# Kernel optimization log

Measured on AMD Instinct MI355X. Metric: run time of the kernel, lower is better.

The kernel has to match this reference:

```python
import jax, jax.numpy as jnp
import numpy as np

B, S, D_MODEL, H = 4, 4096, 1024, 16
HD = D_MODEL // H  # 64
KS = 3             # depthwise conv kernel size
EPS = 1e-6


def dw_causal_conv(x, w, b):
    """Causal depthwise conv over seq. x: [B,S,H,Dk], w: [Dk,KS], b: [Dk].
    Matches Conv1d(groups=d_k, padding=KS-1) followed by cropping the last KS-1."""
    s = x.shape[1]
    xp = jnp.pad(x, ((0, 0), (KS - 1, 0), (0, 0), (0, 0)))
    y = b  # broadcast over [B,S,H,Dk]
    for j in range(KS):
        y = y + w[:, j] * xp[:, j:j + s]
    return y


def feature_map(x):
    return jax.nn.elu(x) + 1.0


def setup_inputs() -> dict:
    key = jax.random.key(0)
    ks = jax.random.split(key, 20)
    sc = 0.02
    inp = {
        'query': jax.random.normal(ks[0], (B, S, D_MODEL), jnp.float32),
        'key':   jax.random.normal(ks[1], (B, S, D_MODEL), jnp.float32),
        'value': jax.random.normal(ks[2], (B, S, D_MODEL), jnp.float32),
        'q_w': jax.random.normal(ks[3], (D_MODEL, D_MODEL), jnp.float32) * sc,
        'q_b': jax.random.normal(ks[4], (D_MODEL,), jnp.float32) * sc,
        'k_w': jax.random.normal(ks[5], (D_MODEL, D_MODEL), jnp.float32) * sc,
        'k_b': jax.random.normal(ks[6], (D_MODEL,), jnp.float32) * sc,
        'v_w': jax.random.normal(ks[7], (D_MODEL, D_MODEL), jnp.float32) * sc,
        'v_b': jax.random.normal(ks[8], (D_MODEL,), jnp.float32) * sc,
        'o_w': jax.random.normal(ks[9], (D_MODEL, D_MODEL), jnp.float32) * sc,
        'o_b': jax.random.normal(ks[10], (D_MODEL,), jnp.float32) * sc,
        'qc_w': jax.random.normal(ks[11], (HD, KS), jnp.float32) * 0.3,
        'qc_b': jax.random.normal(ks[12], (HD,), jnp.float32) * 0.02,
        'kc_w': jax.random.normal(ks[13], (HD, KS), jnp.float32) * 0.3,
        'kc_b': jax.random.normal(ks[14], (HD,), jnp.float32) * 0.02,
        'vc_w': jax.random.normal(ks[15], (HD, KS), jnp.float32) * 0.3,
        'vc_b': jax.random.normal(ks[16], (HD,), jnp.float32) * 0.02,
    }
    return inp


def reference(query, key, value, q_w, q_b, k_w, k_b, v_w, v_b, o_w, o_b,
              qc_w, qc_b, kc_w, kc_b, vc_w, vc_b):
    b, s, _ = query.shape
    q = (query @ q_w.T + q_b).reshape(b, s, H, HD)
    k = (key   @ k_w.T + k_b).reshape(b, s, H, HD)
    v = (value @ v_w.T + v_b).reshape(b, s, H, HD)

    q = feature_map(dw_causal_conv(q, qc_w, qc_b))
    k = feature_map(dw_causal_conv(k, kc_w, kc_b))
    v = dw_causal_conv(v, vc_w, vc_b)

    # linear attention: [B,S,H,D] -> [B,H,S,D]
    Q = q.transpose(0, 2, 1, 3)
    K = k.transpose(0, 2, 1, 3)
    V = v.transpose(0, 2, 1, 3)
    KV = jnp.einsum('bhsd,bhse->bhde', K, V)            # [B,H,D,D]
    Z = 1.0 / jnp.einsum('bhsd,bhd->bhs', Q, K.sum(axis=2) + EPS)
    V_new = jnp.einsum('bhde,bhsd,bhs->bhse', KV, Q, Z)  # [B,H,S,D]

    out = V_new.transpose(0, 2, 1, 3).reshape(b, s, D_MODEL)
    return out @ o_w.T + o_b
```

## Files before the change

### kernel.cpp

```cpp
#include <hip/hip_runtime.h>
#include <hip/hip_bf16.h>
#include <math.h>

#define BB 4
#define SS 4096
#define DM 1024
#define HH 16
#define HD 64
#define NTOK (BB * SS)
#define TSZ ((size_t)NTOK * DM)

typedef _Float16 half8 __attribute__((ext_vector_type(8)));
typedef _Float16 half4v __attribute__((ext_vector_type(4)));
typedef float floatx4 __attribute__((ext_vector_type(4)));

__device__ __forceinline__ void gload16(const void* g, void* l) {
  __builtin_amdgcn_global_load_lds(
      (const __attribute__((address_space(1))) void*)g,
      (__attribute__((address_space(3))) void*)l, 16, 0, 0);
}

#define WAIT4 asm volatile("s_waitcnt vmcnt(4)" ::: "memory")
#define WAIT2 asm volatile("s_waitcnt vmcnt(2)" ::: "memory")
#define WAIT0 asm volatile("s_waitcnt vmcnt(0)" ::: "memory")
#define BARR __builtin_amdgcn_s_barrier()

#define MM3(A_, ah_, al_, bh_, bl_)                                   \
  A_ = __builtin_amdgcn_mfma_f32_16x16x32_f16(ah_, bh_, A_, 0, 0, 0); \
  A_ = __builtin_amdgcn_mfma_f32_16x16x32_f16(ah_, bl_, A_, 0, 0, 0); \
  A_ = __builtin_amdgcn_mfma_f32_16x16x32_f16(al_, bh_, A_, 0, 0, 0)

__device__ __forceinline__ void cvhl(const float4 u0, const float4 u1,
                                     half8& h, half8& l) {
  const float a[8] = {u0.x, u0.y, u0.z, u0.w, u1.x, u1.y, u1.z, u1.w};
#pragma unroll
  for (int e = 0; e < 8; ++e) {
    const _Float16 hh = (_Float16)a[e];
    h[e] = hh;
    l[e] = (_Float16)(a[e] - (float)hh);
  }
}

__global__ __launch_bounds__(256) void split_w4(
    const float* __restrict__ w0, const float* __restrict__ w1,
    const float* __restrict__ w2, const float* __restrict__ w3,
    _Float16* __restrict__ hi, _Float16* __restrict__ lo) {
  const int wi = blockIdx.y;
  const float* src = (wi == 0) ? w0 : (wi == 1) ? w1 : (wi == 2) ? w2 : w3;
  const int i = blockIdx.x * 256 + threadIdx.x;
  const size_t off = ((size_t)wi << 20) >> 2;
  const float4 x = ((const float4*)src)[i];
  half4v h, l;
  h.x = (_Float16)x.x; l.x = (_Float16)(x.x - (float)h.x);
  h.y = (_Float16)x.y; l.y = (_Float16)(x.y - (float)h.y);
  h.z = (_Float16)x.z; l.z = (_Float16)(x.z - (float)h.z);
  h.w = (_Float16)x.w; l.w = (_Float16)(x.w - (float)h.w);
  ((half4v*)hi)[off + i] = h;
  ((half4v*)lo)[off + i] = l;
}

__global__ __launch_bounds__(512, 2) void qkv_gemm8(
    const float* __restrict__ Ak, const float* __restrict__ Av,
    const float* __restrict__ Aq, const _Float16* __restrict__ WhiA,
    const _Float16* __restrict__ WloA, const float* __restrict__ bk,
    const float* __restrict__ bv, const float* __restrict__ bq,
    float* __restrict__ Ck, float* __restrict__ Cv, float* __restrict__ Cq) {
  __shared__ float sA[2][256 * 32];
  __shared__ _Float16 sB[2][256 * 64];

  const int z = blockIdx.z;
  const float* A = (z == 0) ? Ak : (z == 1) ? Av : Aq;
  const float* bias = (z == 0) ? bk : (z == 1) ? bv : bq;
  float* C = (z == 0) ? Ck : (z == 1) ? Cv : Cq;
  const _Float16* Whi = WhiA + ((size_t)z << 20);
  const _Float16* Wlo = WloA + ((size_t)z << 20);

  const int t = threadIdx.x;
  const int wav = t >> 6, lane = t & 63;
  const int wr = wav >> 2, wc = wav & 3;

  const int wg = blockIdx.y * 4 + blockIdx.x;
  const int xcd = wg & 7, cidx = wg >> 3;
  const int bm = ((xcd >> 1) * 16 + (cidx >> 1)) * 256;
  const int bn = ((xcd & 1) * 2 + (cidx & 1)) * 256;

  const int lrow = wav * 8 + (lane >> 3);
  const int cpr = (lane & 7) ^ (lane >> 3);
  const float* pA0 = A + (size_t)(bm + lrow) * DM + cpr * 4;
  const _Float16* pB0 =
      ((cpr < 4) ? Whi : Wlo) + (size_t)(bn + lrow) * DM + (cpr & 3) * 8;
  const int ldsArow = wav * 8 * 32;
  const int ldsBrow = wav * 8 * 64;

#define STA(buf, rb, k0) \
  gload16(pA0 + (size_t)(rb) * DM + (k0), &sA[buf][(rb) * 32 + ldsArow])
#define STB(buf, rb, k0) \
  gload16(pB0 + (size_t)(rb) * DM + (k0), &sB[buf][(rb) * 64 + ldsBrow])

  STA(0, 0, 0); STA(0, 64, 0);
  STB(0, 0, 0); STB(0, 64, 0);
  STB(0, 128, 0); STB(0, 192, 0);
  STA(0, 128, 0); STA(0, 192, 0);

  const int fm = lane & 15;
  const int sw = fm & 7;
  const int kq = lane >> 4;
  int baseA[4], baseB[2];
#pragma unroll
  for (int i = 0; i < 4; ++i) baseA[i] = (wr * 64 + i * 16 + fm) * 32;
#pragma unroll
  for (int j = 0; j < 2; ++j) baseB[j] = (wc * 32 + j * 16 + fm) * 64;
  const int aS0 = ((kq * 2) ^ sw) * 4;
  const int aS1 = ((kq * 2 + 1) ^ sw) * 4;
  const int bSh = (kq ^ sw) * 8;
  const int bSl = ((kq + 4) ^ sw) * 8;

  floatx4 acc[2][4][2][2];
#pragma unroll
  for (int i = 0; i < 2; ++i)
#pragma unroll
    for (int j = 0; j < 4; ++j)
#pragma unroll
      for (int k = 0; k < 2; ++k)
#pragma unroll
        for (int l = 0; l < 2; ++l)
          acc[i][j][k][l] = (floatx4){0.f, 0.f, 0.f, 0.f};

  half8 ah[4], al[4];
  half8 b0h0, b0l0, b0h1, b0l1;
  half8 b1h0, b1l0, b1h1, b1l1;

#define READA_Q(cur_, QM)                                       \
  _Pragma("unroll") for (int i_ = 0; i_ < 4; ++i_) {            \
    const float4 u0_ =                                          \
        *(const float4*)&sA[cur_][baseA[i_] + (QM) * 4096 + aS0]; \
    const float4 u1_ =                                          \
        *(const float4*)&sA[cur_][baseA[i_] + (QM) * 4096 + aS1]; \
    cvhl(u0_, u1_, ah[i_], al[i_]);                             \
  }

#define RB_Q(cur_, QN, H0, L0, H1, L1)                          \
  H0 = *(const half8*)&sB[cur_][baseB[0] + (QN) * 8192 + bSh];  \
  L0 = *(const half8*)&sB[cur_][baseB[0] + (QN) * 8192 + bSl];  \
  H1 = *(const half8*)&sB[cur_][baseB[1] + (QN) * 8192 + bSh];  \
  L1 = *(const half8*)&sB[cur_][baseB[1] + (QN) * 8192 + bSl]

#define MFMACL(QM, QN, H0, L0, H1, L1)                          \
  __builtin_amdgcn_s_setprio(1);                                \
  _Pragma("unroll") for (int i_ = 0; i_ < 4; ++i_) {            \
    MM3(acc[QM][i_][QN][0], ah[i_], al[i_], H0, L0);            \
    MM3(acc[QM][i_][QN][1], ah[i_], al[i_], H1, L1);            \
  }                                                             \
  __builtin_amdgcn_s_setprio(0)

  for (int tt = 0; tt < 31; ++tt) {
    const int cur = tt & 1, nxt = cur ^ 1;
    const int k1 = tt * 32 + 32;
    WAIT4; BARR;
    READA_Q(cur, 0);
    RB_Q(cur, 0, b0h0, b0l0, b0h1, b0l1);
    STA(nxt, 0, k1); STA(nxt, 64, k1);
    MFMACL(0, 0, b0h0, b0l0, b0h1, b0l1);
    BARR;
    WAIT4; BARR;
    RB_Q(cur, 1, b1h0, b1l0, b1h1, b1l1);
    STB(nxt, 0, k1); STB(nxt, 64, k1);
    MFMACL(0, 1, b1h0, b1l0, b1h1, b1l1);
    BARR;
    WAIT4; BARR;
    READA_Q(cur, 1);
    STB(nxt, 128, k1); STB(nxt, 192, k1);
    MFMACL(1, 0, b0h0, b0l0, b0h1, b0l1);
    BARR;
    STA(nxt, 128, k1); STA(nxt, 192, k1);
    MFMACL(1, 1, b1h0, b1l0, b1h1, b1l1);
  }
  WAIT4; BARR;
  READA_Q(1, 0);
  RB_Q(1, 0, b0h0, b0l0, b0h1, b0l1);
  MFMACL(0, 0, b0h0, b0l0, b0h1, b0l1);
  BARR;
  WAIT2; BARR;
  RB_Q(1, 1, b1h0, b1l0, b1h1, b1l1);
  MFMACL(0, 1, b1h0, b1l0, b1h1, b1l1);
  BARR;
  WAIT0; BARR;
  READA_Q(1, 1);
  MFMACL(1, 0, b0h0, b0l0, b0h1, b0l1);
  MFMACL(1, 1, b1h0, b1l0, b1h1, b1l1);

  const int cr = (lane >> 4) * 4;
#pragma unroll
  for (int qm = 0; qm < 2; ++qm)
#pragma unroll
    for (int i = 0; i < 4; ++i) {
      const int grow = bm + qm * 128 + wr * 64 + i * 16 + cr;
#pragma unroll
      for (int qn = 0; qn < 2; ++qn)
#pragma unroll
        for (int j = 0; j < 2; ++j) {
          const int gcol = bn + qn * 128 + wc * 32 + j * 16 + fm;
          const float bo = bias[gcol];
#pragma unroll
          for (int r = 0; r < 4; ++r)
            C[(size_t)(grow + r) * DM + gcol] = acc[qm][i][qn][j][r] + bo;
        }
    }
#undef STA
#undef STB
#undef READA_Q
#undef RB_Q
#undef MFMACL
}

__global__ __launch_bounds__(512, 2) void o_gemm8(
    const _Float16* __restrict__ Ahi, const _Float16* __restrict__ Alo,
    const _Float16* __restrict__ Whi, const _Float16* __restrict__ Wlo,
    const float* __restrict__ bias, float* __restrict__ C) {
  __shared__ _Float16 sA[2][256 * 64];
  __shared__ _Float16 sB[2][256 * 64];

  const int t = threadIdx.x;
  const int wav = t >> 6, lane = t & 63;
  const int wr = wav >> 2, wc = wav & 3;

  const int wg = blockIdx.y * 4 + blockIdx.x;
  const int xcd = wg & 7, cidx = wg >> 3;
  const int bm = ((xcd >> 1) * 16 + (cidx >> 1)) * 256;
  const int bn = ((xcd & 1) * 2 + (cidx & 1)) * 256;

  const int lrow = wav * 8 + (lane >> 3);
  const int cpr = (lane & 7) ^ (lane >> 3);
  const _Float16* pA0 =
      ((cpr < 4) ? Ahi : Alo) + (size_t)(bm + lrow) * DM + (cpr & 3) * 8;
  const _Float16* pB0 =
      ((cpr < 4) ? Whi : Wlo) + (size_t)(bn + lrow) * DM + (cpr & 3) * 8;
  const int ldsRow = wav * 8 * 64;

#define STAO(buf, rb, k0) \
  gload16(pA0 + (size_t)(rb) * DM + (k0), &sA[buf][(rb) * 64 + ldsRow])
#define STBO(buf, rb, k0) \
  gload16(pB0 + (size_t)(rb) * DM + (k0), &sB[buf][(rb) * 64 + ldsRow])

  STAO(0, 0, 0); STAO(0, 64, 0);
  STBO(0, 0, 0); STBO(0, 64, 0);
  STBO(0, 128, 0); STBO(0, 192, 0);
  STAO(0, 128, 0); STAO(0, 192, 0);

  const int fm = lane & 15;
  const int sw = fm & 7;
  const int kq = lane >> 4;
  int baseA[4], baseB[2];
#pragma unroll
  for (int i = 0; i < 4; ++i) baseA[i] = (wr * 64 + i * 16 + fm) * 64;
#pragma unroll
  for (int j = 0; j < 2; ++j) baseB[j] = (wc * 32 + j * 16 + fm) * 64;
  const int bSh = (kq ^ sw) * 8;
  const int bSl = ((kq + 4) ^ sw) * 8;

  floatx4 acc[2][4][2][2];
#pragma unroll
  for (int i = 0; i < 2; ++i)
#pragma unroll
    for (int j = 0; j < 4; ++j)
#pragma unroll
      for (int k = 0; k < 2; ++k)
#pragma unroll
        for (int l = 0; l < 2; ++l)
          acc[i][j][k][l] = (floatx4){0.f, 0.f, 0.f, 0.f};

  half8 ah[4], al[4];
  half8 b0h0, b0l0, b0h1, b0l1;
  half8 b1h0, b1l0, b1h1, b1l1;

#define READA_O(cur_, QM)                                                 \
  _Pragma("unroll") for (int i_ = 0; i_ < 4; ++i_) {                      \
    ah[i_] = *(const half8*)&sA[cur_][baseA[i_] + (QM) * 8192 + bSh];     \
    al[i_] = *(const half8*)&sA[cur_][baseA[i_] + (QM) * 8192 + bSl];     \
  }

#define RB_O(cur_, QN, H0, L0, H1, L1)                          \
  H0 = *(const half8*)&sB[cur_][baseB[0] + (QN) * 8192 + bSh];  \
  L0 = *(const half8*)&sB[cur_][baseB[0] + (QN) * 8192 + bSl];  \
  H1 = *(const half8*)&sB[cur_][baseB[1] + (QN) * 8192 + bSh];  \
  L1 = *(const half8*)&sB[cur_][baseB[1] + (QN) * 8192 + bSl]

#define MFMACLO(QM, QN, H0, L0, H1, L1)                         \
  __builtin_amdgcn_s_setprio(1);                                \
  _Pragma("unroll") for (int i_ = 0; i_ < 4; ++i_) {            \
    MM3(acc[QM][i_][QN][0], ah[i_], al[i_], H0, L0);            \
    MM3(acc[QM][i_][QN][1], ah[i_], al[i_], H1, L1);            \
  }                                                             \
  __builtin_amdgcn_s_setprio(0)

  for (int tt = 0; tt < 31; ++tt) {
    const int cur = tt & 1, nxt = cur ^ 1;
    const int k1 = tt * 32 + 32;
    WAIT4; BARR;
    READA_O(cur, 0);
    RB_O(cur, 0, b0h0, b0l0, b0h1, b0l1);
    STAO(nxt, 0, k1); STAO(nxt, 64, k1);
    MFMACLO(0, 0, b0h0, b0l0, b0h1, b0l1);
    BARR;
    WAIT4; BARR;
    RB_O(cur, 1, b1h0, b1l0, b1h1, b1l1);
    STBO(nxt, 0, k1); STBO(nxt, 64, k1);
    MFMACLO(0, 1, b1h0, b1l0, b1h1, b1l1);
    BARR;
    WAIT4; BARR;
    READA_O(cur, 1);
    STBO(nxt, 128, k1); STBO(nxt, 192, k1);
    MFMACLO(1, 0, b0h0, b0l0, b0h1, b0l1);
    BARR;
    STAO(nxt, 128, k1); STAO(nxt, 192, k1);
    MFMACLO(1, 1, b1h0, b1l0, b1h1, b1l1);
  }
  WAIT4; BARR;
  READA_O(1, 0);
  RB_O(1, 0, b0h0, b0l0, b0h1, b0l1);
  MFMACLO(0, 0, b0h0, b0l0, b0h1, b0l1);
  BARR;
  WAIT2; BARR;
  RB_O(1, 1, b1h0, b1l0, b1h1, b1l1);
  MFMACLO(0, 1, b1h0, b1l0, b1h1, b1l1);
  BARR;
  WAIT0; BARR;
  READA_O(1, 1);
  MFMACLO(1, 0, b0h0, b0l0, b0h1, b0l1);
  MFMACLO(1, 1, b1h0, b1l0, b1h1, b1l1);

  const int cr = (lane >> 4) * 4;
#pragma unroll
  for (int qm = 0; qm < 2; ++qm)
#pragma unroll
    for (int i = 0; i < 4; ++i) {
      const int grow = bm + qm * 128 + wr * 64 + i * 16 + cr;
#pragma unroll
      for (int qn = 0; qn < 2; ++qn)
#pragma unroll
        for (int j = 0; j < 2; ++j) {
          const int gcol = bn + qn * 128 + wc * 32 + j * 16 + fm;
          const float bo = bias[gcol];
#pragma unroll
          for (int r = 0; r < 4; ++r)
            C[(size_t)(grow + r) * DM + gcol] = acc[qm][i][qn][j][r] + bo;
        }
    }
#undef STAO
#undef STBO
#undef READA_O
#undef RB_O
#undef MFMACLO
}

__global__ __launch_bounds__(256) void kv_accum_conv(
    const float* __restrict__ Kg, const float* __restrict__ Vg,
    const float* __restrict__ kc_w, const float* __restrict__ kc_b,
    const float* __restrict__ vc_w, const float* __restrict__ vc_b,
    float* __restrict__ KVp, float* __restrict__ Ksp) {
  const int bh = blockIdx.x;
  const int b = bh >> 4, h = bh & 15;
  const int chunk = blockIdx.y;
  const int s0 = chunk * 256;
  const int t = threadIdx.x;
  const int w = t >> 6, lane = t & 63;
  __shared__ float Kr[34][64], Vr[34][64];
  __shared__ float Kc[32][64], Vc[32][64];
  __shared__ float kw0[64], kw1[64], kw2[64], kb_[64];
  __shared__ float vw0[64], vw1[64], vw2[64], vb_[64];

  if (t < 64) {
    kw0[t] = kc_w[t * 3 + 0]; kw1[t] = kc_w[t * 3 + 1]; kw2[t] = kc_w[t * 3 + 2];
    vw0[t] = vc_w[t * 3 + 0]; vw1[t] = vc_w[t * 3 + 1]; vw2[t] = vc_w[t * 3 + 2];
    kb_[t] = kc_b[t]; vb_[t] = vc_b[t];
  }

  const int d0 = w * 16 + (lane >> 4) * 4;
  const int e0 = (lane & 15) * 4;
  float acc[4][4];
#pragma unroll
  for (int i = 0; i < 4; ++i)
#pragma unroll
    for (int j = 0; j < 4; ++j) acc[i][j] = 0.f;
  float4 ks = make_float4(0.f, 0.f, 0.f, 0.f);
  const size_t gbase = (size_t)b * SS * DM + h * HD;

  float4 kpre[3], vpre[3];
#define KVFETCH(cc)                                                        \
  _Pragma("unroll") for (int u = 0; u < 3; ++u) {                          \
    const int idx = t + u * 256;                                           \
    if (idx < 544) {                                                       \
      const int row = idx >> 4, col = (idx & 15) * 4;                      \
      const int s = s0 + (cc) - 2 + row;                                   \
      float4 k4 = make_float4(0.f, 0.f, 0.f, 0.f);                         \
      float4 v4 = make_float4(0.f, 0.f, 0.f, 0.f);                         \
      if (s >= 0) {                                                        \
        k4 = *(const float4*)&Kg[gbase + (size_t)s * DM + col];            \
        v4 = *(const float4*)&Vg[gbase + (size_t)s * DM + col];            \
      }                                                                    \
      kpre[u] = k4; vpre[u] = v4;                                          \
    }                                                                      \
  }
#define KVWRITE                                                            \
  _Pragma("unroll") for (int u = 0; u < 3; ++u) {                          \
    const int idx = t + u * 256;                                           \
    if (idx < 544) {                                                       \
      const int row = idx >> 4, col = (idx & 15) * 4;                      \
      *(float4*)&Kr[row][col] = kpre[u];                                   \
      *(float4*)&Vr[row][col] = vpre[u];                                   \
    }                                                                      \
  }

  KVFETCH(0);
  for (int c = 0; c < 256; c += 32) {
    __syncthreads();
    KVWRITE;
    __syncthreads();
    for (int idx = t; idx < 2048; idx += 256) {
      const int row = idx >> 6, dd = idx & 63;
      float yk = kb_[dd] + kw0[dd] * Kr[row][dd] + kw1[dd] * Kr[row + 1][dd] +
                 kw2[dd] * Kr[row + 2][dd];
      Kc[row][dd] = (yk > 0.f) ? (yk + 1.f) : expf(yk);
      Vc[row][dd] = vb_[dd] + vw0[dd] * Vr[row][dd] + vw1[dd] * Vr[row + 1][dd] +
                    vw2[dd] * Vr[row + 2][dd];
    }
    if (c + 32 < 256) KVFETCH(c + 32);
    __syncthreads();
#pragma unroll 2
    for (int ss = 0; ss < 32; ++ss) {
      const float4 k4 = *(const float4*)&Kc[ss][d0];
      const float4 v4 = *(const float4*)&Vc[ss][e0];
      ks.x += k4.x; ks.y += k4.y; ks.z += k4.z; ks.w += k4.w;
      const float kk[4] = {k4.x, k4.y, k4.z, k4.w};
      const float vv[4] = {v4.x, v4.y, v4.z, v4.w};
#pragma unroll
      for (int i = 0; i < 4; ++i)
#pragma unroll
        for (int j = 0; j < 4; ++j) acc[i][j] = fmaf(kk[i], vv[j], acc[i][j]);
    }
  }
  float* kvp = &KVp[((size_t)(bh * 16 + chunk)) * 4096];
#pragma unroll
  for (int i = 0; i < 4; ++i) {
    float4 o = make_float4(acc[i][0], acc[i][1], acc[i][2], acc[i][3]);
    *(float4*)&kvp[(d0 + i) * 64 + e0] = o;
  }
  if ((lane & 15) == 0) {
    float* kp = &Ksp[(bh * 16 + chunk) * 64 + d0];
    kp[0] = ks.x; kp[1] = ks.y; kp[2] = ks.z; kp[3] = ks.w;
  }
#undef KVFETCH
#undef KVWRITE
}

__global__ __launch_bounds__(256) void kv_reduce(
    const float* __restrict__ KVp, const float* __restrict__ Ksp,
    float* __restrict__ KV, float* __restrict__ Ksum) {
  const int bh = blockIdx.x;
  const int t = threadIdx.x;
  for (int i = t; i < 4096; i += 256) {
    float s = 0.f;
#pragma unroll
    for (int c = 0; c < 16; ++c) s += KVp[((size_t)(bh * 16 + c)) * 4096 + i];
    KV[(size_t)bh * 4096 + i] = s;
  }
  if (t < 64) {
    float s = 1e-6f;
#pragma unroll
    for (int c = 0; c < 16; ++c) s += Ksp[(bh * 16 + c) * 64 + t];
    Ksum[bh * 64 + t] = s;
  }
}

__global__ __launch_bounds__(256) void attn_apply_conv(
    const float* __restrict__ Qg, const float* __restrict__ KV,
    const float* __restrict__ Ksum, const float* __restrict__ qc_w,
    const float* __restrict__ qc_b, _Float16* __restrict__ OHi,
    _Float16* __restrict__ OLo) {
  const int bh = blockIdx.x;
  const int b = bh >> 4, h = bh & 15;
  const int s0 = blockIdx.y * 64;
  const int t = threadIdx.x;
  const int w = t >> 6, lane = t & 63;
  __shared__ float Qr[66][64];
  __shared__ float QsT[64][68];
  __shared__ float KVs[64][64];
  __shared__ float pden[64][4];
  __shared__ float kse[64];
  __shared__ float qw0[64], qw1[64], qw2[64], qb_[64];
  const size_t gbase = (size_t)b * SS * DM + h * HD;

  for (int idx = t; idx < 1056; idx += 256) {
    const int row = idx >> 4, col = (idx & 15) * 4;
    const int s = s0 - 2 + row;
    float4 q4 = make_float4(0.f, 0.f, 0.f, 0.f);
    if (s >= 0) q4 = *(const float4*)&Qg[gbase + (size_t)s * DM + col];
    *(float4*)&Qr[row][col] = q4;
  }
  for (int idx = t; idx < 1024; idx += 256) {
    const int row = idx >> 4, col = (idx & 15) * 4;
    *(float4*)&KVs[row][col] = *(const float4*)&KV[(size_t)bh * 4096 + row * 64 + col];
  }
  if (t < 64) {
    kse[t] = Ksum[bh * 64 + t];
    qw0[t] = qc_w[t * 3 + 0]; qw1[t] = qc_w[t * 3 + 1]; qw2[t] = qc_w[t * 3 + 2];
    qb_[t] = qc_b[t];
  }
  __syncthreads();

  {
    const int crow = t >> 2;
    const int db = (t & 3) * 16;
    float denp = 0.f;
#pragma unroll
    for (int q = 0; q < 4; ++q) {
      const float4 xm2 = *(const float4*)&Qr[crow][db + q * 4];
      const float4 xm1 = *(const float4*)&Qr[crow + 1][db + q * 4];
      const float4 xc0 = *(const float4*)&Qr[crow + 2][db + q * 4];
      const float a2[4] = {xm2.x, xm2.y, xm2.z, xm2.w};
      const float a1[4] = {xm1.x, xm1.y, xm1.z, xm1.w};
      const float a0[4] = {xc0.x, xc0.y, xc0.z, xc0.w};
#pragma unroll
      for (int e = 0; e < 4; ++e) {
        const int dd = db + q * 4 + e;
        float y = qb_[dd] + qw0[dd] * a2[e] + qw1[dd] * a1[e] + qw2[dd] * a0[e];
        y = (y > 0.f) ? (y + 1.f) : expf(y);
        denp = fmaf(y, kse[dd], denp);
        QsT[dd][crow] = y;
      }
    }
    pden[crow][t & 3] = denp;
  }
  __syncthreads();

  const int sl0 = w * 16 + (lane >> 4) * 4;
  const int e0 = (lane & 15) * 4;
  float acc[4][4];
#pragma unroll
  for (int i = 0; i < 4; ++i)
#pragma unroll
    for (int j = 0; j < 4; ++j) acc[i][j] = 0.f;
#pragma unroll 2
  for (int d = 0; d < 64; ++d) {
    const float4 q4 = *(const float4*)&QsT[d][sl0];
    const float4 v4 = *(const float4*)&KVs[d][e0];
    const float qq[4] = {q4.x, q4.y, q4.z, q4.w};
    const float vv[4] = {v4.x, v4.y, v4.z, v4.w};
#pragma unroll
    for (int i = 0; i < 4; ++i)
#pragma unroll
      for (int j = 0; j < 4; ++j) acc[i][j] = fmaf(qq[i], vv[j], acc[i][j]);
  }
#pragma unroll
  for (int i = 0; i < 4; ++i) {
    const float4 pd = *(const float4*)&pden[sl0 + i][0];
    const float zz = 1.0f / (pd.x + pd.y + pd.z + pd.w);
    const float o[4] = {acc[i][0] * zz, acc[i][1] * zz, acc[i][2] * zz,
                        acc[i][3] * zz};
    half4v hh, ll;
#pragma unroll
    for (int e = 0; e < 4; ++e) {
      const _Float16 hv = (_Float16)o[e];
      hh[e] = hv;
      ll[e] = (_Float16)(o[e] - (float)hv);
    }
    const size_t base = gbase + (size_t)(s0 + sl0 + i) * DM + e0;
    *(half4v*)&OHi[base] = hh;
    *(half4v*)&OLo[base] = ll;
  }
}

extern "C" void kernel_launch(void* const* d_in, const int* in_sizes, int n_in,
                              void* d_out, int out_size, void* d_ws, size_t ws_size,
                              hipStream_t stream) {
  const float* query = (const float*)d_in[0];
  const float* key   = (const float*)d_in[1];
  const float* value = (const float*)d_in[2];
  const float* q_w = (const float*)d_in[3];
  const float* q_b = (const float*)d_in[4];
  const float* k_w = (const float*)d_in[5];
  const float* k_b = (const float*)d_in[6];
  const float* v_w = (const float*)d_in[7];
  const float* v_b = (const float*)d_in[8];
  const float* o_w = (const float*)d_in[9];
  const float* o_b = (const float*)d_in[10];
  const float* qc_w = (const float*)d_in[11];
  const float* qc_b = (const float*)d_in[12];
  const float* kc_w = (const float*)d_in[13];
  const float* kc_b = (const float*)d_in[14];
  const float* vc_w = (const float*)d_in[15];
  const float* vc_b = (const float*)d_in[16];
  float* out = (float*)d_out;

  float* ws = (float*)d_ws;
  float* buf0 = ws;
  float* buf1 = ws + TSZ;
  float* buf2 = ws + 2 * TSZ;
  _Float16* Whi = (_Float16*)(ws + 3 * TSZ);
  _Float16* Wlo = Whi + 4 * (1 << 20);
  float* KVp  = (float*)(Wlo + 4 * (1 << 20));
  float* Ksp  = KVp + (size_t)64 * 16 * 4096;
  float* KV   = Ksp + 64 * 16 * 64;
  float* Ksum = KV + (size_t)64 * 4096;

  _Float16* WhiO = Whi + 3 * (1 << 20);
  _Float16* WloO = Wlo + 3 * (1 << 20);
  _Float16* OHi = (_Float16*)buf0;
  _Float16* OLo = OHi + TSZ;

  const int nW4 = DM * DM / 4;

  split_w4<<<dim3(nW4 / 256, 4), 256, 0, stream>>>(k_w, v_w, q_w, o_w, Whi, Wlo);

  qkv_gemm8<<<dim3(4, 64, 3), 512, 0, stream>>>(
      key, value, query, Whi, Wlo, k_b, v_b, q_b, buf0, buf1, buf2);

  kv_accum_conv<<<dim3(64, 16), 256, 0, stream>>>(buf0, buf1, kc_w, kc_b, vc_w,
                                                  vc_b, KVp, Ksp);
  kv_reduce<<<64, 256, 0, stream>>>(KVp, Ksp, KV, Ksum);

  attn_apply_conv<<<dim3(64, 64), 256, 0, stream>>>(buf2, KV, Ksum, qc_w, qc_b,
                                                    OHi, OLo);

  o_gemm8<<<dim3(4, 64), 512, 0, stream>>>(OHi, OLo, WhiO, WloO, o_b, out);
}
```

Measured before the change: 722.5 us.

## Simplify GEMM pipelining to one wait per k-step and drop KV register prefetch

Both fp16-split GEMMs replace the fine-grained interleaved staging, with partial vmcnt waits and several barriers per k-step, by one full wait and barrier. After that barrier all next-tile loads are issued at once, then the full MFMA cluster runs. The kv_accum_conv kernel drops its register prefetch of the next K/V chunk and loads it synchronously instead. This cuts barrier count and register pressure, but gives up finer overlap of global loads with compute and exposes load latency in the conv kernel.

```diff
diff --git a/kernel.cpp b/kernel.cpp
--- a/kernel.cpp
+++ b/kernel.cpp
@@ -20,8 +20,6 @@
       (__attribute__((address_space(3))) void*)l, 16, 0, 0);
 }
 
-#define WAIT4 asm volatile("s_waitcnt vmcnt(4)" ::: "memory")
-#define WAIT2 asm volatile("s_waitcnt vmcnt(2)" ::: "memory")
 #define WAIT0 asm volatile("s_waitcnt vmcnt(0)" ::: "memory")
 #define BARR __builtin_amdgcn_s_barrier()
 
@@ -59,7 +57,7 @@
   ((half4v*)lo)[off + i] = l;
 }
 
-__global__ __launch_bounds__(512, 2) void qkv_gemm8(
+__global__ __launch_bounds__(512, 2) void qkv_gemm9(
     const float* __restrict__ Ak, const float* __restrict__ Av,
     const float* __restrict__ Aq, const _Float16* __restrict__ WhiA,
     const _Float16* __restrict__ WloA, const float* __restrict__ bk,
@@ -97,10 +95,13 @@
 #define STB(buf, rb, k0) \
   gload16(pB0 + (size_t)(rb) * DM + (k0), &sB[buf][(rb) * 64 + ldsBrow])
 
-  STA(0, 0, 0); STA(0, 64, 0);
-  STB(0, 0, 0); STB(0, 64, 0);
-  STB(0, 128, 0); STB(0, 192, 0);
-  STA(0, 128, 0); STA(0, 192, 0);
+#define STAGE_ALL(buf, k0)                          \
+  STA(buf, 0, k0); STA(buf, 64, k0);                \
+  STA(buf, 128, k0); STA(buf, 192, k0);             \
+  STB(buf, 0, k0); STB(buf, 64, k0);                \
+  STB(buf, 128, k0); STB(buf, 192, k0)
+
+  STAGE_ALL(0, 0);
 
   const int fm = lane & 15;
   const int sw = fm & 7;
@@ -145,49 +146,36 @@
   H1 = *(const half8*)&sB[cur_][baseB[1] + (QN) * 8192 + bSh];  \
   L1 = *(const half8*)&sB[cur_][baseB[1] + (QN) * 8192 + bSl]
 
-#define MFMACL(QM, QN, H0, L0, H1, L1)                          \
+#define MFMACL(QM)                                              \
   __builtin_amdgcn_s_setprio(1);                                \
   _Pragma("unroll") for (int i_ = 0; i_ < 4; ++i_) {            \
-    MM3(acc[QM][i_][QN][0], ah[i_], al[i_], H0, L0);            \
-    MM3(acc[QM][i_][QN][1], ah[i_], al[i_], H1, L1);            \
+    MM3(acc[QM][i_][0][0], ah[i_], al[i_], b0h0, b0l0);         \
+    MM3(acc[QM][i_][0][1], ah[i_], al[i_], b0h1, b0l1);         \
+    MM3(acc[QM][i_][1][0], ah[i_], al[i_], b1h0, b1l0);         \
+    MM3(acc[QM][i_][1][1], ah[i_], al[i_], b1h1, b1l1);         \
   }                                                             \
   __builtin_amdgcn_s_setprio(0)
 
   for (int tt = 0; tt < 31; ++tt) {
     const int cur = tt & 1, nxt = cur ^ 1;
-    const int k1 = tt * 32 + 32;
-    WAIT4; BARR;
+    const int k1 = (tt + 1) * 32;
+    WAIT0;
+    BARR;
+    STAGE_ALL(nxt, k1);
     READA_Q(cur, 0);
     RB_Q(cur, 0, b0h0, b0l0, b0h1, b0l1);
-    STA(nxt, 0, k1); STA(nxt, 64, k1);
-    MFMACL(0, 0, b0h0, b0l0, b0h1, b0l1);
-    BARR;
-    WAIT4; BARR;
     RB_Q(cur, 1, b1h0, b1l0, b1h1, b1l1);
-    STB(nxt, 0, k1); STB(nxt, 64, k1);
-    MFMACL(0, 1, b1h0, b1l0, b1h1, b1l1);
-    BARR;
-    WAIT4; BARR;
+    MFMACL(0);
     READA_Q(cur, 1);
-    STB(nxt, 128, k1); STB(nxt, 192, k1);
-    MFMACL(1, 0, b0h0, b0l0, b0h1, b0l1);
-    BARR;
-    STA(nxt, 128, k1); STA(nxt, 192, k1);
-    MFMACL(1, 1, b1h0, b1l0, b1h1, b1l1);
-  }
-  WAIT4; BARR;
+    MFMACL(1);
+  }
+  WAIT0; BARR;
   READA_Q(1, 0);
   RB_Q(1, 0, b0h0, b0l0, b0h1, b0l1);
-  MFMACL(0, 0, b0h0, b0l0, b0h1, b0l1);
-  BARR;
-  WAIT2; BARR;
   RB_Q(1, 1, b1h0, b1l0, b1h1, b1l1);
-  MFMACL(0, 1, b1h0, b1l0, b1h1, b1l1);
-  BARR;
-  WAIT0; BARR;
+  MFMACL(0);
   READA_Q(1, 1);
-  MFMACL(1, 0, b0h0, b0l0, b0h1, b0l1);
-  MFMACL(1, 1, b1h0, b1l0, b1h1, b1l1);
+  MFMACL(1);
 
   const int cr = (lane >> 4) * 4;
 #pragma unroll
@@ -208,12 +196,13 @@
     }
 #undef STA
 #undef STB
+#undef STAGE_ALL
 #undef READA_Q
 #undef RB_Q
 #undef MFMACL
 }
 
-__global__ __launch_bounds__(512, 2) void o_gemm8(
+__global__ __launch_bounds__(512, 2) void o_gemm9(
     const _Float16* __restrict__ Ahi, const _Float16* __restrict__ Alo,
     const _Float16* __restrict__ Whi, const _Float16* __restrict__ Wlo,
     const float* __restrict__ bias, float* __restrict__ C) {
@@ -242,10 +231,13 @@
 #define STBO(buf, rb, k0) \
   gload16(pB0 + (size_t)(rb) * DM + (k0), &sB[buf][(rb) * 64 + ldsRow])
 
-  STAO(0, 0, 0); STAO(0, 64, 0);
-  STBO(0, 0, 0); STBO(0, 64, 0);
-  STBO(0, 128, 0); STBO(0, 192, 0);
-  STAO(0, 128, 0); STAO(0, 192, 0);
+#define STAGE_ALLO(buf, k0)                         \
+  STAO(buf, 0, k0); STAO(buf, 64, k0);              \
+  STAO(buf, 128, k0); STAO(buf, 192, k0);           \
+  STBO(buf, 0, k0); STBO(buf, 64, k0);              \
+  STBO(buf, 128, k0); STBO(buf, 192, k0)
+
+  STAGE_ALLO(0, 0);
 
   const int fm = lane & 15;
   const int sw = fm & 7;
@@ -285,49 +277,36 @@
   H1 = *(const half8*)&sB[cur_][baseB[1] + (QN) * 8192 + bSh];  \
   L1 = *(const half8*)&sB[cur_][baseB[1] + (QN) * 8192 + bSl]
 
-#define MFMACLO(QM, QN, H0, L0, H1, L1)                         \
+#define MFMACLO(QM)                                             \
   __builtin_amdgcn_s_setprio(1);                                \
   _Pragma("unroll") for (int i_ = 0; i_ < 4; ++i_) {            \
-    MM3(acc[QM][i_][QN][0], ah[i_], al[i_], H0, L0);            \
-    MM3(acc[QM][i_][QN][1], ah[i_], al[i_], H1, L1);            \
+    MM3(acc[QM][i_][0][0], ah[i_], al[i_], b0h0, b0l0);         \
+    MM3(acc[QM][i_][0][1], ah[i_], al[i_], b0h1, b0l1);         \
+    MM3(acc[QM][i_][1][0], ah[i_], al[i_], b1h0, b1l0);         \
+    MM3(acc[QM][i_][1][1], ah[i_], al[i_], b1h1, b1l1);         \
   }                                                             \
   __builtin_amdgcn_s_setprio(0)
 
   for (int tt = 0; tt < 31; ++tt) {
     const int cur = tt & 1, nxt = cur ^ 1;
-    const int k1 = tt * 32 + 32;
-    WAIT4; BARR;
+    const int k1 = (tt + 1) * 32;
+    WAIT0;
+    BARR;
+    STAGE_ALLO(nxt, k1);
     READA_O(cur, 0);
     RB_O(cur, 0, b0h0, b0l0, b0h1, b0l1);
-    STAO(nxt, 0, k1); STAO(nxt, 64, k1);
-    MFMACLO(0, 0, b0h0, b0l0, b0h1, b0l1);
-    BARR;
-    WAIT4; BARR;
     RB_O(cur, 1, b1h0, b1l0, b1h1, b1l1);
-    STBO(nxt, 0, k1); STBO(nxt, 64, k1);
-    MFMACLO(0, 1, b1h0, b1l0, b1h1, b1l1);
-    BARR;
-    WAIT4; BARR;
+    MFMACLO(0);
     READA_O(cur, 1);
-    STBO(nxt, 128, k1); STBO(nxt, 192, k1);
-    MFMACLO(1, 0, b0h0, b0l0, b0h1, b0l1);
-    BARR;
-    STAO(nxt, 128, k1); STAO(nxt, 192, k1);
-    MFMACLO(1, 1, b1h0, b1l0, b1h1, b1l1);
-  }
-  WAIT4; BARR;
+    MFMACLO(1);
+  }
+  WAIT0; BARR;
   READA_O(1, 0);
   RB_O(1, 0, b0h0, b0l0, b0h1, b0l1);
-  MFMACLO(0, 0, b0h0, b0l0, b0h1, b0l1);
-  BARR;
-  WAIT2; BARR;
   RB_O(1, 1, b1h0, b1l0, b1h1, b1l1);
-  MFMACLO(0, 1, b1h0, b1l0, b1h1, b1l1);
-  BARR;
-  WAIT0; BARR;
+  MFMACLO(0);
   READA_O(1, 1);
-  MFMACLO(1, 0, b0h0, b0l0, b0h1, b0l1);
-  MFMACLO(1, 1, b1h0, b1l0, b1h1, b1l1);
+  MFMACLO(1);
 
   const int cr = (lane >> 4) * 4;
 #pragma unroll
@@ -348,6 +327,7 @@
     }
 #undef STAO
 #undef STBO
+#undef STAGE_ALLO
 #undef READA_O
 #undef RB_O
 #undef MFMACLO
@@ -385,36 +365,20 @@
   float4 ks = make_float4(0.f, 0.f, 0.f, 0.f);
   const size_t gbase = (size_t)b * SS * DM + h * HD;
 
-  float4 kpre[3], vpre[3];
-#define KVFETCH(cc)                                                        \
-  _Pragma("unroll") for (int u = 0; u < 3; ++u) {                          \
-    const int idx = t + u * 256;                                           \
-    if (idx < 544) {                                                       \
-      const int row = idx >> 4, col = (idx & 15) * 4;                      \
-      const int s = s0 + (cc) - 2 + row;                                   \
-      float4 k4 = make_float4(0.f, 0.f, 0.f, 0.f);                         \
-      float4 v4 = make_float4(0.f, 0.f, 0.f, 0.f);                         \
-      if (s >= 0) {                                                        \
-        k4 = *(const float4*)&Kg[gbase + (size_t)s * DM + col];            \
-        v4 = *(const float4*)&Vg[gbase + (size_t)s * DM + col];            \
-      }                                                                    \
-      kpre[u] = k4; vpre[u] = v4;                                          \
-    }                                                                      \
-  }
-#define KVWRITE                                                            \
-  _Pragma("unroll") for (int u = 0; u < 3; ++u) {                          \
-    const int idx = t + u * 256;                                           \
-    if (idx < 544) {                                                       \
-      const int row = idx >> 4, col = (idx & 15) * 4;                      \
-      *(float4*)&Kr[row][col] = kpre[u];                                   \
-      *(float4*)&Vr[row][col] = vpre[u];                                   \
-    }                                                                      \
-  }
-
-  KVFETCH(0);
   for (int c = 0; c < 256; c += 32) {
     __syncthreads();
-    KVWRITE;
+    for (int idx = t; idx < 544; idx += 256) {
+      const int row = idx >> 4, col = (idx & 15) * 4;
+      const int s = s0 + c - 2 + row;
+      float4 k4 = make_float4(0.f, 0.f, 0.f, 0.f);
+      float4 v4 = make_float4(0.f, 0.f, 0.f, 0.f);
+      if (s >= 0) {
+        k4 = *(const float4*)&Kg[gbase + (size_t)s * DM + col];
+        v4 = *(const float4*)&Vg[gbase + (size_t)s * DM + col];
+      }
+      *(float4*)&Kr[row][col] = k4;
+      *(float4*)&Vr[row][col] = v4;
+    }
     __syncthreads();
     for (int idx = t; idx < 2048; idx += 256) {
       const int row = idx >> 6, dd = idx & 63;
@@ -424,7 +388,6 @@
       Vc[row][dd] = vb_[dd] + vw0[dd] * Vr[row][dd] + vw1[dd] * Vr[row + 1][dd] +
                     vw2[dd] * Vr[row + 2][dd];
     }
-    if (c + 32 < 256) KVFETCH(c + 32);
     __syncthreads();
 #pragma unroll 2
     for (int ss = 0; ss < 32; ++ss) {
@@ -449,8 +412,6 @@
     float* kp = &Ksp[(bh * 16 + chunk) * 64 + d0];
     kp[0] = ks.x; kp[1] = ks.y; kp[2] = ks.z; kp[3] = ks.w;
   }
-#undef KVFETCH
-#undef KVWRITE
 }
 
 __global__ __launch_bounds__(256) void kv_reduce(
@@ -612,7 +573,7 @@
 
   split_w4<<<dim3(nW4 / 256, 4), 256, 0, stream>>>(k_w, v_w, q_w, o_w, Whi, Wlo);
 
-  qkv_gemm8<<<dim3(4, 64, 3), 512, 0, stream>>>(
+  qkv_gemm9<<<dim3(4, 64, 3), 512, 0, stream>>>(
       key, value, query, Whi, Wlo, k_b, v_b, q_b, buf0, buf1, buf2);
 
   kv_accum_conv<<<dim3(64, 16), 256, 0, stream>>>(buf0, buf1, kc_w, kc_b, vc_w,
@@ -622,5 +583,5 @@
   attn_apply_conv<<<dim3(64, 64), 256, 0, stream>>>(buf2, KV, Ksum, qc_w, qc_b,
                                                     OHi, OLo);
 
-  o_gemm8<<<dim3(4, 64), 512, 0, stream>>>(OHi, OLo, WhiO, WloO, o_b, out);
-}
+  o_gemm9<<<dim3(4, 64), 512, 0, stream>>>(OHi, OLo, WhiO, WloO, o_b, out);
+}
```

After: 787.7 us. 9.0% more time.
